# Performance work log

Hardware: AMD Instinct MI355X
Metric: run time of the kernel (lower is better)

Reference implementation:

```python
import jax, jax.numpy as jnp
import numpy as np

N_NODES = 100000
N_EDGES = 1600000
IN_DIM = 256
OUT_DIM = 64
LEAKY_SLOPE = 0.01  # torch F.leaky_relu default


def setup_inputs() -> dict:
    key = jax.random.key(0)
    k1, k2, k3, k4, k5 = jax.random.split(key, 5)
    h = jax.random.normal(k1, (N_NODES, IN_DIM), dtype=jnp.float32)
    W_fc = jax.random.normal(k2, (IN_DIM, OUT_DIM), dtype=jnp.float32) * (1.0 / np.sqrt(IN_DIM))
    a_attn = jax.random.normal(k3, (2 * OUT_DIM,), dtype=jnp.float32) * (1.0 / np.sqrt(2 * OUT_DIM))
    edge_src = jax.random.randint(k4, (N_EDGES,), 0, N_NODES, dtype=jnp.int32)
    edge_dst = jax.random.randint(k5, (N_EDGES,), 0, N_NODES, dtype=jnp.int32)
    return {"h": h, "W_fc": W_fc, "a_attn": a_attn, "edge_src": edge_src, "edge_dst": edge_dst}


def reference(h, W_fc, a_attn, edge_src, edge_dst):
    # z = fc(h)  (no bias)
    z = h @ W_fc                                   # [N, D]
    # edge attention: leaky_relu(concat(z_src, z_dst) @ a)
    # split a into src/dst halves -> node-level projections (same math, no concat)
    el = z @ a_attn[:OUT_DIM]                      # [N]
    er = z @ a_attn[OUT_DIM:]                      # [N]
    e = jax.nn.leaky_relu(el[edge_src] + er[edge_dst], negative_slope=LEAKY_SLOPE)  # [E]
    # segment softmax over destination-node mailboxes
    m = jax.ops.segment_max(e, edge_dst, num_segments=N_NODES)   # [N]
    ex = jnp.exp(e - m[edge_dst])                                # [E]
    s = jax.ops.segment_sum(ex, edge_dst, num_segments=N_NODES)  # [N]
    alpha = ex / s[edge_dst]                                     # [E]
    # weighted scatter-sum of neighbor features
    h_out = jax.ops.segment_sum(alpha[:, None] * z[edge_src], edge_dst, num_segments=N_NODES)  # [N, D]
    # heads != 1 branch: ELU (dropout = 0 in eval)
    return jax.nn.elu(h_out)
```

## Files before the change

kernel.cpp:

```cpp
#include <hip/hip_runtime.h>
#include <hip/hip_bf16.h>

#define IN_DIM 256
#define OUT_DIM 64
#define CHUNK 8192
#define BSH 8
#define P2CAP 6144

typedef short bf16x8 __attribute__((ext_vector_type(8)));
typedef float f32x4 __attribute__((ext_vector_type(4)));

__device__ inline unsigned short f2bf(float x) {
  unsigned int u = __float_as_uint(x);
  return (unsigned short)((u + 0x7FFFu + ((u >> 16) & 1u)) >> 16);
}

#define GLOAD_LDS16(gp, lp)                                                        \
  __builtin_amdgcn_global_load_lds(                                                \
      (const __attribute__((address_space(1))) unsigned int*)(gp),                 \
      (__attribute__((address_space(3))) unsigned int*)(lp), 16, 0, 0)

__global__ __launch_bounds__(256) void k_prep(const float* __restrict__ W,
                                              unsigned short* __restrict__ Wbf,
                                              int* __restrict__ gcur) {
  int f = blockIdx.x * 256 + threadIdx.x;
  if (f < 512) gcur[f] = f * P2CAP;
  int kc = f >> 8, ct = (f >> 6) & 3, q = (f >> 4) & 3, nq = f & 15;
  int col = ct * 16 + nq, k0 = kc * 32 + q * 8;
  unsigned short v[8];
#pragma unroll
  for (int j = 0; j < 8; ++j) v[j] = f2bf(W[(size_t)(k0 + j) * OUT_DIM + col]);
  *(uint4*)(Wbf + (size_t)f * 8) = *(uint4*)v;
}

__global__ __launch_bounds__(256, 4) void k_gemm(const float* __restrict__ h,
                                                 const unsigned short* __restrict__ Wbf,
                                                 const float* __restrict__ a,
                                                 unsigned short* __restrict__ zb,
                                                 float* __restrict__ el,
                                                 float* __restrict__ er, int n) {
  __shared__ __align__(16) unsigned short Wlds[16384];
  const int t = threadIdx.x;
  const int w = t >> 6, lane = t & 63, nq = lane & 15, q = lane >> 4;

#pragma unroll
  for (int i = 0; i < 8; ++i) {
    const char* gp = (const char*)Wbf + (size_t)(i * 256 + t) * 16;
    char* lp = (char*)Wlds + (i * 4096 + w * 1024);
    GLOAD_LDS16(gp, lp);
  }
  __syncthreads();

  const int tile = blockIdx.x * 4 + w;
  const int arow = tile * 16 + nq;
  const float* Ap = h + (size_t)min(arow, n - 1) * IN_DIM + q * 8;

  float4 alo[8], ahi[8];
#pragma unroll
  for (int kc = 0; kc < 8; ++kc) {
    alo[kc] = *(const float4*)(Ap + kc * 32);
    ahi[kc] = *(const float4*)(Ap + kc * 32 + 4);
  }

  f32x4 acc[4];
#pragma unroll
  for (int ct = 0; ct < 4; ++ct) acc[ct] = (f32x4){0.f, 0.f, 0.f, 0.f};

#pragma unroll
  for (int kc = 0; kc < 8; ++kc) {
    bf16x8 af;
    af[0] = (short)f2bf(alo[kc].x); af[1] = (short)f2bf(alo[kc].y);
    af[2] = (short)f2bf(alo[kc].z); af[3] = (short)f2bf(alo[kc].w);
    af[4] = (short)f2bf(ahi[kc].x); af[5] = (short)f2bf(ahi[kc].y);
    af[6] = (short)f2bf(ahi[kc].z); af[7] = (short)f2bf(ahi[kc].w);
#pragma unroll
    for (int ct = 0; ct < 4; ++ct) {
      bf16x8 wfr = *(const bf16x8*)&Wlds[(size_t)((kc * 4 + ct) * 64 + lane) * 8];
      acc[ct] = __builtin_amdgcn_mfma_f32_16x16x32_bf16(af, wfr, acc[ct], 0, 0, 0);
    }
  }

  float a1[4], a2[4];
#pragma unroll
  for (int ct = 0; ct < 4; ++ct) {
    a1[ct] = a[ct * 16 + nq];
    a2[ct] = a[OUT_DIM + ct * 16 + nq];
  }
#pragma unroll
  for (int r = 0; r < 4; ++r) {
    int orow = tile * 16 + q * 4 + r;
    float p1 = 0.f, p2 = 0.f;
#pragma unroll
    for (int ct = 0; ct < 4; ++ct) {
      float v = acc[ct][r];
      p1 += v * a1[ct];
      p2 += v * a2[ct];
      if (orow < n) zb[(size_t)orow * OUT_DIM + ct * 16 + nq] = f2bf(v);
    }
    p1 += __shfl_xor(p1, 1); p1 += __shfl_xor(p1, 2);
    p1 += __shfl_xor(p1, 4); p1 += __shfl_xor(p1, 8);
    p2 += __shfl_xor(p2, 1); p2 += __shfl_xor(p2, 2);
    p2 += __shfl_xor(p2, 4); p2 += __shfl_xor(p2, 8);
    if (orow < n && nq == 0) { el[orow] = p1; er[orow] = p2; }
  }
}

__global__ __launch_bounds__(512) void k_part(const int* __restrict__ src,
                                              const int* __restrict__ dst,
                                              int* __restrict__ gcur,
                                              int* __restrict__ pairs, int E,
                                              int nbuck) {
  __shared__ int hist[512];
  __shared__ int excl[512];
  __shared__ int cur[512];
  __shared__ int rbase[512];
  __shared__ int stage[CHUNK];
  __shared__ unsigned short sbk[CHUNK];
  __shared__ int wtot[8];
  const int t = threadIdx.x, b = blockIdx.x;
  const int beg = b * CHUNK;
  const int cnt = min(CHUNK, E - beg);

  hist[t] = 0;
  __syncthreads();

  int dv[16], sv[16];
#pragma unroll
  for (int k = 0; k < 16; ++k) {
    int i = k * 512 + t;
    dv[k] = -1;
    if (i < cnt) {
      dv[k] = dst[beg + i];
      sv[k] = src[beg + i];
      atomicAdd(&hist[dv[k] >> BSH], 1);
    }
  }
  __syncthreads();

  {
    int v = hist[t];
    int lane = t & 63, w = t >> 6;
    int incl = v;
    for (int o = 1; o < 64; o <<= 1) {
      int u = __shfl_up(incl, o);
      if (lane >= o) incl += u;
    }
    if (lane == 63) wtot[w] = incl;
    __syncthreads();
    int woff = 0;
    for (int i = 0; i < 8; ++i)
      if (i < w) woff += wtot[i];
    int ex = woff + incl - v;
    excl[t] = ex;
    cur[t] = ex;
    if (t < nbuck && v > 0) rbase[t] = atomicAdd(&gcur[t], v);
  }
  __syncthreads();

#pragma unroll
  for (int k = 0; k < 16; ++k) {
    if (dv[k] >= 0) {
      int bk = dv[k] >> BSH;
      int r = atomicAdd(&cur[bk], 1);
      stage[r] = ((dv[k] & ((1 << BSH) - 1)) << 24) | sv[k];
      sbk[r] = (unsigned short)bk;
    }
  }
  __syncthreads();

  for (int i = t; i < cnt; i += 512) {
    int bk = sbk[i];
    int idx = rbase[bk] + (i - excl[bk]);
    if (idx < (bk + 1) * P2CAP) pairs[idx] = stage[i];
  }
}

__global__ __launch_bounds__(1024) void k_p2agg(const int* __restrict__ pairs,
                                                const int* __restrict__ gcur,
                                                const float* __restrict__ el,
                                                const float* __restrict__ er,
                                                const unsigned short* __restrict__ zb,
                                                float* __restrict__ out, int n) {
  __shared__ int deg[256];
  __shared__ int loff[257];
  __shared__ int cur[256];
  __shared__ int stage[P2CAP];
  __shared__ int wtot[4];
  const int t = threadIdx.x, b = blockIdx.x;
  const int beg = b * P2CAP;
  const int cnt = min(gcur[b] - beg, P2CAP);

  if (t < 256) deg[t] = 0;
  __syncthreads();

  int pv[6];
#pragma unroll
  for (int k = 0; k < 6; ++k) {
    int i = k * 1024 + t;
    pv[k] = 0;
    if (i < cnt) {
      pv[k] = pairs[beg + i];
      atomicAdd(&deg[((unsigned)pv[k]) >> 24], 1);
    }
  }
  __syncthreads();

  int v = 0, inc = 0;
  const int lane = t & 63, w = t >> 6;
  if (t < 256) {
    v = deg[t];
    inc = v;
    for (int o = 1; o < 64; o <<= 1) {
      int u = __shfl_up(inc, o);
      if (lane >= o) inc += u;
    }
    if (lane == 63) wtot[w] = inc;
  }
  __syncthreads();
  if (t < 256) {
    int woff = 0;
    for (int i = 0; i < 4; ++i)
      if (i < w) woff += wtot[i];
    int ex = woff + inc - v;
    loff[t] = ex;
    cur[t] = ex;
    if (t == 255) loff[256] = ex + v;
  }
  __syncthreads();

#pragma unroll
  for (int k = 0; k < 6; ++k) {
    int i = k * 1024 + t;
    if (i < cnt) {
      int r = atomicAdd(&cur[((unsigned)pv[k]) >> 24], 1);
      if (r < P2CAP) stage[r] = pv[k] & 0xFFFFFF;
    }
  }
  __syncthreads();

  const int g = t >> 4;
  const int cq = (t & 15) * 4;
#pragma unroll
  for (int round = 0; round < 4; ++round) {
    int nl = round * 64 + g;
    int node = (b << BSH) + nl;
    if (node >= n) continue;
    int jb = loff[nl], je = loff[nl + 1];
    float erd = er[node];
    float ax = 0.f, ay = 0.f, az = 0.f, aw = 0.f, ssum = 0.f;
    int j = jb;
    for (; j + 4 <= je; j += 4) {
      int s0 = stage[j], s1 = stage[j + 1], s2 = stage[j + 2], s3 = stage[j + 3];
      uint2 z0 = *(const uint2*)(zb + (s0 << 6) + cq);
      uint2 z1 = *(const uint2*)(zb + (s1 << 6) + cq);
      uint2 z2 = *(const uint2*)(zb + (s2 << 6) + cq);
      uint2 z3 = *(const uint2*)(zb + (s3 << 6) + cq);
      float x0 = el[s0] + erd, x1 = el[s1] + erd;
      float x2 = el[s2] + erd, x3 = el[s3] + erd;
      x0 = x0 > 0.f ? x0 : 0.01f * x0;
      x1 = x1 > 0.f ? x1 : 0.01f * x1;
      x2 = x2 > 0.f ? x2 : 0.01f * x2;
      x3 = x3 > 0.f ? x3 : 0.01f * x3;
      float e0 = __expf(x0), e1 = __expf(x1), e2 = __expf(x2), e3 = __expf(x3);
      ssum += (e0 + e1) + (e2 + e3);
      ax += e0 * __uint_as_float(z0.x << 16) + e1 * __uint_as_float(z1.x << 16) +
            e2 * __uint_as_float(z2.x << 16) + e3 * __uint_as_float(z3.x << 16);
      ay += e0 * __uint_as_float(z0.x & 0xFFFF0000u) + e1 * __uint_as_float(z1.x & 0xFFFF0000u) +
            e2 * __uint_as_float(z2.x & 0xFFFF0000u) + e3 * __uint_as_float(z3.x & 0xFFFF0000u);
      az += e0 * __uint_as_float(z0.y << 16) + e1 * __uint_as_float(z1.y << 16) +
            e2 * __uint_as_float(z2.y << 16) + e3 * __uint_as_float(z3.y << 16);
      aw += e0 * __uint_as_float(z0.y & 0xFFFF0000u) + e1 * __uint_as_float(z1.y & 0xFFFF0000u) +
            e2 * __uint_as_float(z2.y & 0xFFFF0000u) + e3 * __uint_as_float(z3.y & 0xFFFF0000u);
    }
    for (; j < je; ++j) {
      int s = stage[j];
      uint2 zv = *(const uint2*)(zb + (s << 6) + cq);
      float x = el[s] + erd;
      x = x > 0.f ? x : 0.01f * x;
      float ex = __expf(x);
      ssum += ex;
      ax += ex * __uint_as_float(zv.x << 16);
      ay += ex * __uint_as_float(zv.x & 0xFFFF0000u);
      az += ex * __uint_as_float(zv.y << 16);
      aw += ex * __uint_as_float(zv.y & 0xFFFF0000u);
    }
    float4 o = make_float4(0.f, 0.f, 0.f, 0.f);
    if (je > jb) {
      float inv = 1.f / ssum;
      ax *= inv; ay *= inv; az *= inv; aw *= inv;
      o.x = ax > 0.f ? ax : __expf(ax) - 1.f;
      o.y = ay > 0.f ? ay : __expf(ay) - 1.f;
      o.z = az > 0.f ? az : __expf(az) - 1.f;
      o.w = aw > 0.f ? aw : __expf(aw) - 1.f;
    }
    *(float4*)(out + ((size_t)node << 6) + cq) = o;
  }
}

extern "C" void kernel_launch(void* const* d_in, const int* in_sizes, int n_in,
                              void* d_out, int out_size, void* d_ws, size_t ws_size,
                              hipStream_t stream) {
  const float* h = (const float*)d_in[0];
  const float* W = (const float*)d_in[1];
  const float* a = (const float*)d_in[2];
  const int* src = (const int*)d_in[3];
  const int* dst = (const int*)d_in[4];
  const int n = in_sizes[0] / IN_DIM;
  const int E = in_sizes[3];
  float* out = (float*)d_out;

  const int b1 = (E + CHUNK - 1) / CHUNK;
  const int nbuck = (n + (1 << BSH) - 1) >> BSH;

  char* ws = (char*)d_ws;
  auto alloc = [&](size_t bytes) {
    char* p = ws;
    ws += (bytes + 15) & ~(size_t)15;
    return p;
  };
  unsigned short* Wbf = (unsigned short*)alloc(16384 * 2);
  unsigned short* zb = (unsigned short*)alloc((size_t)n * OUT_DIM * 2);
  float* el = (float*)alloc((size_t)n * 4);
  float* er = (float*)alloc((size_t)n * 4);
  int* gcur = (int*)alloc(512 * 4);
  int* pairs = (int*)alloc((size_t)(nbuck + 1) * P2CAP * 4);

  k_prep<<<8, 256, 0, stream>>>(W, Wbf, gcur);
  k_gemm<<<(n + 63) / 64, 256, 0, stream>>>(h, Wbf, a, zb, el, er, n);
  k_part<<<b1, 512, 0, stream>>>(src, dst, gcur, pairs, E, nbuck);
  k_p2agg<<<nbuck, 1024, 0, stream>>>(pairs, gcur, el, er, zb, out, n);
}
```

Baseline: 234.3 us.

## Merge GEMM and edge partition kernels into one interleaved launch

Fuses the projection GEMM kernel and the edge bucket-partition kernel into a single launch. Every fifth block does partitioning, on a smaller 4096-edge chunk with 256 threads, and the remaining blocks do GEMM tiles. The goal is to overlap the compute-bound GEMM with the memory- and atomic-bound partition and to save one launch. In exchange, the partition blocks run with half the threads and smaller chunks, so the global atomics on the bucket cursors double, and the shared memory footprint is sized for both roles.

After: 230.5 us. Within noise of the previous version (-1.6%).

```diff
diff --git a/kernel.cpp b/kernel.cpp
--- a/kernel.cpp
+++ b/kernel.cpp
@@ -3,7 +3,7 @@
 
 #define IN_DIM 256
 #define OUT_DIM 64
-#define CHUNK 8192
+#define PCHUNK 4096
 #define BSH 8
 #define P2CAP 6144
 
@@ -33,14 +33,99 @@
   *(uint4*)(Wbf + (size_t)f * 8) = *(uint4*)v;
 }
 
-__global__ __launch_bounds__(256, 4) void k_gemm(const float* __restrict__ h,
-                                                 const unsigned short* __restrict__ Wbf,
-                                                 const float* __restrict__ a,
-                                                 unsigned short* __restrict__ zb,
-                                                 float* __restrict__ el,
-                                                 float* __restrict__ er, int n) {
-  __shared__ __align__(16) unsigned short Wlds[16384];
+__global__ __launch_bounds__(256, 4) void k_gp(const float* __restrict__ h,
+                                               const unsigned short* __restrict__ Wbf,
+                                               const float* __restrict__ a,
+                                               unsigned short* __restrict__ zb,
+                                               float* __restrict__ el,
+                                               float* __restrict__ er, int n,
+                                               const int* __restrict__ src,
+                                               const int* __restrict__ dst,
+                                               int* __restrict__ gcur,
+                                               int* __restrict__ pairs, int E,
+                                               int nbuck, int nchunk) {
+  __shared__ __align__(16) char smem[32800];
   const int t = threadIdx.x;
+  const int bid = blockIdx.x;
+
+  const bool ispart = (bid % 5 == 0) && (bid / 5 < nchunk);
+
+  if (ispart) {
+    int* s_hist = (int*)smem;
+    int* s_excl = s_hist + 512;
+    int* s_cur = s_excl + 512;
+    int* s_rbase = s_cur + 512;
+    int* s_stage = s_rbase + 512;
+    unsigned short* s_sbk = (unsigned short*)(s_stage + PCHUNK);
+    int* s_wtot = (int*)(s_sbk + PCHUNK);
+
+    const int pid = bid / 5;
+    const int beg = pid * PCHUNK;
+    const int cnt = min(PCHUNK, E - beg);
+
+    s_hist[t] = 0;
+    s_hist[t + 256] = 0;
+    __syncthreads();
+
+    int dv[16], sv[16];
+#pragma unroll
+    for (int k = 0; k < 16; ++k) {
+      int i = k * 256 + t;
+      dv[k] = -1;
+      if (i < cnt) {
+        dv[k] = dst[beg + i];
+        sv[k] = src[beg + i];
+        atomicAdd(&s_hist[dv[k] >> BSH], 1);
+      }
+    }
+    __syncthreads();
+
+    {
+      int d0 = s_hist[2 * t], d1 = s_hist[2 * t + 1];
+      int tsum = d0 + d1;
+      int lane = t & 63, w = t >> 6;
+      int incl = tsum;
+      for (int o = 1; o < 64; o <<= 1) {
+        int u = __shfl_up(incl, o);
+        if (lane >= o) incl += u;
+      }
+      if (lane == 63) s_wtot[w] = incl;
+      __syncthreads();
+      int woff = 0;
+      for (int i = 0; i < 4; ++i)
+        if (i < w) woff += s_wtot[i];
+      int ex = woff + incl - tsum;
+      s_excl[2 * t] = ex;
+      s_cur[2 * t] = ex;
+      s_excl[2 * t + 1] = ex + d0;
+      s_cur[2 * t + 1] = ex + d0;
+      if (2 * t < nbuck && d0 > 0) s_rbase[2 * t] = atomicAdd(&gcur[2 * t], d0);
+      if (2 * t + 1 < nbuck && d1 > 0)
+        s_rbase[2 * t + 1] = atomicAdd(&gcur[2 * t + 1], d1);
+    }
+    __syncthreads();
+
+#pragma unroll
+    for (int k = 0; k < 16; ++k) {
+      if (dv[k] >= 0) {
+        int bk = dv[k] >> BSH;
+        int r = atomicAdd(&s_cur[bk], 1);
+        s_stage[r] = ((dv[k] & ((1 << BSH) - 1)) << 24) | sv[k];
+        s_sbk[r] = (unsigned short)bk;
+      }
+    }
+    __syncthreads();
+
+    for (int i = t; i < cnt; i += 256) {
+      int bk = s_sbk[i];
+      int idx = s_rbase[bk] + (i - s_excl[bk]);
+      if (idx < (bk + 1) * P2CAP) pairs[idx] = s_stage[i];
+    }
+    return;
+  }
+
+  unsigned short* Wlds = (unsigned short*)smem;
+  const int gid = bid - min(bid / 5 + 1, nchunk);
   const int w = t >> 6, lane = t & 63, nq = lane & 15, q = lane >> 4;
 
 #pragma unroll
@@ -51,7 +136,7 @@
   }
   __syncthreads();
 
-  const int tile = blockIdx.x * 4 + w;
+  const int tile = gid * 4 + w;
   const int arow = tile * 16 + nq;
   const float* Ap = h + (size_t)min(arow, n - 1) * IN_DIM + q * 8;
 
@@ -102,76 +187,6 @@
     p2 += __shfl_xor(p2, 1); p2 += __shfl_xor(p2, 2);
     p2 += __shfl_xor(p2, 4); p2 += __shfl_xor(p2, 8);
     if (orow < n && nq == 0) { el[orow] = p1; er[orow] = p2; }
-  }
-}
-
-__global__ __launch_bounds__(512) void k_part(const int* __restrict__ src,
-                                              const int* __restrict__ dst,
-                                              int* __restrict__ gcur,
-                                              int* __restrict__ pairs, int E,
-                                              int nbuck) {
-  __shared__ int hist[512];
-  __shared__ int excl[512];
-  __shared__ int cur[512];
-  __shared__ int rbase[512];
-  __shared__ int stage[CHUNK];
-  __shared__ unsigned short sbk[CHUNK];
-  __shared__ int wtot[8];
-  const int t = threadIdx.x, b = blockIdx.x;
-  const int beg = b * CHUNK;
-  const int cnt = min(CHUNK, E - beg);
-
-  hist[t] = 0;
-  __syncthreads();
-
-  int dv[16], sv[16];
-#pragma unroll
-  for (int k = 0; k < 16; ++k) {
-    int i = k * 512 + t;
-    dv[k] = -1;
-    if (i < cnt) {
-      dv[k] = dst[beg + i];
-      sv[k] = src[beg + i];
-      atomicAdd(&hist[dv[k] >> BSH], 1);
-    }
-  }
-  __syncthreads();
-
-  {
-    int v = hist[t];
-    int lane = t & 63, w = t >> 6;
-    int incl = v;
-    for (int o = 1; o < 64; o <<= 1) {
-      int u = __shfl_up(incl, o);
-      if (lane >= o) incl += u;
-    }
-    if (lane == 63) wtot[w] = incl;
-    __syncthreads();
-    int woff = 0;
-    for (int i = 0; i < 8; ++i)
-      if (i < w) woff += wtot[i];
-    int ex = woff + incl - v;
-    excl[t] = ex;
-    cur[t] = ex;
-    if (t < nbuck && v > 0) rbase[t] = atomicAdd(&gcur[t], v);
-  }
-  __syncthreads();
-
-#pragma unroll
-  for (int k = 0; k < 16; ++k) {
-    if (dv[k] >= 0) {
-      int bk = dv[k] >> BSH;
-      int r = atomicAdd(&cur[bk], 1);
-      stage[r] = ((dv[k] & ((1 << BSH) - 1)) << 24) | sv[k];
-      sbk[r] = (unsigned short)bk;
-    }
-  }
-  __syncthreads();
-
-  for (int i = t; i < cnt; i += 512) {
-    int bk = sbk[i];
-    int idx = rbase[bk] + (i - excl[bk]);
-    if (idx < (bk + 1) * P2CAP) pairs[idx] = stage[i];
   }
 }
 
@@ -309,8 +324,10 @@
   const int E = in_sizes[3];
   float* out = (float*)d_out;
 
-  const int b1 = (E + CHUNK - 1) / CHUNK;
+  const int nchunk = (E + PCHUNK - 1) / PCHUNK;
   const int nbuck = (n + (1 << BSH) - 1) >> BSH;
+  const int gemmb = (n + 63) / 64;
+  const int grid = gemmb + nchunk;
 
   char* ws = (char*)d_ws;
   auto alloc = [&](size_t bytes) {
@@ -326,7 +343,7 @@
   int* pairs = (int*)alloc((size_t)(nbuck + 1) * P2CAP * 4);
 
   k_prep<<<8, 256, 0, stream>>>(W, Wbf, gcur);
-  k_gemm<<<(n + 63) / 64, 256, 0, stream>>>(h, Wbf, a, zb, el, er, n);
-  k_part<<<b1, 512, 0, stream>>>(src, dst, gcur, pairs, E, nbuck);
+  k_gp<<<grid, 256, 0, stream>>>(h, Wbf, a, zb, el, er, n, src, dst, gcur, pairs,
+                                 E, nbuck, nchunk);
   k_p2agg<<<nbuck, 1024, 0, stream>>>(pairs, gcur, el, er, zb, out, n);
 }
```
